# Kernel tuning notes

Measured on AMD Instinct MI355X. Metric: run time of the kernel, lower is better.

## Reference

```python
import jax, jax.numpy as jnp
import numpy as np

N_NODES = 100_000
N_POS = 1_600_000
N_NEG = 1_600_000
HID = 32


def gcn_conv(x, edge_index, W, b, num_nodes):
    """torch_geometric GCNConv: add self-loops, symmetric norm, linear-first, bias after agg."""
    xl = x @ W  # [N, out]
    loops = jnp.arange(num_nodes, dtype=edge_index.dtype)
    src = jnp.concatenate([edge_index[0], loops])
    dst = jnp.concatenate([edge_index[1], loops])
    deg = jax.ops.segment_sum(jnp.ones_like(dst, dtype=xl.dtype), dst, num_segments=num_nodes)
    dinv = jnp.where(deg > 0, jax.lax.rsqrt(deg), 0.0)
    norm = dinv[src] * dinv[dst]  # [E+N]
    out = jax.ops.segment_sum(norm[:, None] * xl[src], dst, num_segments=num_nodes)
    return out + b


def setup_inputs() -> dict:
    key = jax.random.key(0)
    ks = jax.random.split(key, 8)
    x = jax.random.normal(ks[0], (N_NODES, HID), dtype=jnp.float32)
    pos_edge_index = jax.random.randint(ks[1], (2, N_POS), 0, N_NODES, dtype=jnp.int32)
    neg_edge_index = jax.random.randint(ks[2], (2, N_NEG), 0, N_NODES, dtype=jnp.int32)
    s = lambda fan_in: 1.0 / np.sqrt(fan_in)
    W1 = jax.random.normal(ks[3], (HID, 128), dtype=jnp.float32) * s(HID)
    b1 = jnp.zeros((128,), jnp.float32)
    W2 = jax.random.normal(ks[4], (128, HID), dtype=jnp.float32) * s(128)
    b2 = jnp.zeros((HID,), jnp.float32)
    Wm1 = jax.random.normal(ks[5], (2 * HID, HID), dtype=jnp.float32) * s(2 * HID)
    bm1 = jnp.zeros((HID,), jnp.float32)
    Wm2 = jax.random.normal(ks[6], (HID, 2), dtype=jnp.float32) * s(HID)
    bm2 = jnp.zeros((2,), jnp.float32)
    return dict(x=x, pos_edge_index=pos_edge_index, neg_edge_index=neg_edge_index,
                W1=W1, b1=b1, W2=W2, b2=b2, Wm1=Wm1, bm1=bm1, Wm2=Wm2, bm2=bm2)


def reference(x, pos_edge_index, neg_edge_index, W1, b1, W2, b2, Wm1, bm1, Wm2, bm2):
    n = x.shape[0]
    h = jax.nn.relu(gcn_conv(x, pos_edge_index, W1, b1, n))
    h = jax.nn.relu(gcn_conv(h, pos_edge_index, W2, b2, n))  # [N, hid]
    ei = jnp.concatenate([pos_edge_index, neg_edge_index], axis=-1)  # [2, Ep+En]
    feat = jnp.concatenate([h[ei[0]], h[ei[1]]], axis=1)  # [E, 2*hid]
    out = jax.nn.relu(feat @ Wm1 + bm1) @ Wm2 + bm2  # [E, 2]
    return out
```

## Files before the change

kernel.cpp:

```cpp
#include <hip/hip_runtime.h>
#include <hip/hip_fp16.h>


#define HIDN 32
#define SCAN_B 256

struct __align__(8) Half4 { __half2 a, b; };

__global__ void k_deg(const int* __restrict__ dst, int E, int* __restrict__ deg) {
    int e = blockIdx.x * blockDim.x + threadIdx.x;
    if (e < E) atomicAdd(&deg[__builtin_nontemporal_load(dst + e)], 1);
}

__global__ void k_scan1(const int* __restrict__ deg, int N,
                        int* __restrict__ part, int* __restrict__ bsum,
                        float* __restrict__ dinv,
                        const float4* __restrict__ x4, Half4* __restrict__ xs4) {
    __shared__ int sh[SCAN_B];
    __shared__ float dsh[SCAN_B];
    int t = threadIdx.x, i = blockIdx.x * SCAN_B + t;
    int v = (i < N) ? deg[i] : 0;
    float dv = rsqrtf((float)(v + 1));
    if (i < N) dinv[i] = dv;
    dsh[t] = dv;
    sh[t] = v; __syncthreads();
    for (int o = 1; o < SCAN_B; o <<= 1) {
        int a = (t >= o) ? sh[t - o] : 0;
        __syncthreads();
        sh[t] += a;
        __syncthreads();
    }
    if (i < N) part[i] = sh[t] - v;
    if (t == SCAN_B - 1) bsum[blockIdx.x] = sh[t];
#pragma unroll
    for (int it = 0; it < 8; ++it) {
        int q = it * SCAN_B + t;
        int g = blockIdx.x * (SCAN_B * 8) + q;
        if (g < N * 8) {
            float w = dsh[q >> 3];
            float4 a = x4[g];
            Half4 hv;
            hv.a = __floats2half2_rn(a.x * w, a.y * w);
            hv.b = __floats2half2_rn(a.z * w, a.w * w);
            xs4[g] = hv;
        }
    }
}

__global__ void k_scan2(int* __restrict__ bsum, int nb) {
    __shared__ int sh[1024];
    int t = threadIdx.x;
    int v = (t < nb) ? bsum[t] : 0;
    sh[t] = v; __syncthreads();
    for (int o = 1; o < 1024; o <<= 1) {
        int a = (t >= o) ? sh[t - o] : 0;
        __syncthreads();
        sh[t] += a;
        __syncthreads();
    }
    if (t < nb) bsum[t] = sh[t] - v;
}

__global__ void k_scan3(const int* __restrict__ part, const int* __restrict__ bsum,
                        int N, int E, int* __restrict__ rowptr, int* __restrict__ cursor) {
    int i = blockIdx.x * blockDim.x + threadIdx.x;
    if (i < N) {
        int r = part[i] + bsum[i / SCAN_B];
        rowptr[i] = r;
        cursor[i] = r;
    }
    if (i == N) rowptr[N] = E;
}

__global__ void k_fill_sweep(const int* __restrict__ src, const int* __restrict__ dst,
                             int E, int lo, int hi,
                             int* __restrict__ cursor, int* __restrict__ csr) {
    int e = blockIdx.x * blockDim.x + threadIdx.x;
    if (e >= E) return;
    int d = __builtin_nontemporal_load(dst + e);
    if (d >= lo && d < hi) {
        int j = atomicAdd(&cursor[d], 1);
        csr[j] = __builtin_nontemporal_load(src + e);
    }
}

#define ADD8(raw)                                        \
    {                                                    \
        const __half2* _h = (const __half2*)&(raw);      \
        float2 _f;                                       \
        _f = __half22float2(_h[0]); a0 += _f.x; a1 += _f.y; \
        _f = __half22float2(_h[1]); a2 += _f.x; a3 += _f.y; \
        _f = __half22float2(_h[2]); a4 += _f.x; a5 += _f.y; \
        _f = __half22float2(_h[3]); a6 += _f.x; a7 += _f.y; \
    }

__global__ void k_gather_h(const float4* __restrict__ tbl, const float* __restrict__ dinv,
                           const int* __restrict__ rowptr, const int* __restrict__ csr,
                           int N, float4* __restrict__ out) {
    int t = blockIdx.x * blockDim.x + threadIdx.x;
    if (t >= N * 4) return;
    int i = t >> 2, c = t & 3;
    float di = dinv[i];
    float a0 = 0.f, a1 = 0.f, a2 = 0.f, a3 = 0.f;
    float a4 = 0.f, a5 = 0.f, a6 = 0.f, a7 = 0.f;
    {
        float4 raw = tbl[(size_t)i * 4 + c];
        ADD8(raw);
    }
    int p = rowptr[i], end = rowptr[i + 1];
    for (; p + 3 < end; p += 4) {
        int s0 = __builtin_nontemporal_load(csr + p);
        int s1 = __builtin_nontemporal_load(csr + p + 1);
        int s2 = __builtin_nontemporal_load(csr + p + 2);
        int s3 = __builtin_nontemporal_load(csr + p + 3);
        float4 r0 = tbl[(size_t)s0 * 4 + c];
        float4 r1 = tbl[(size_t)s1 * 4 + c];
        float4 r2 = tbl[(size_t)s2 * 4 + c];
        float4 r3 = tbl[(size_t)s3 * 4 + c];
        ADD8(r0); ADD8(r1); ADD8(r2); ADD8(r3);
    }
    for (; p < end; ++p) {
        float4 r = tbl[(size_t)__builtin_nontemporal_load(csr + p) * 4 + c];
        ADD8(r);
    }
    out[(size_t)i * 8 + 2 * c]     = make_float4(a0 * di, a1 * di, a2 * di, a3 * di);
    out[(size_t)i * 8 + 2 * c + 1] = make_float4(a4 * di, a5 * di, a6 * di, a7 * di);
}

__global__ __launch_bounds__(256) void k_mlp1(
        const float4* __restrict__ agg1, const float* __restrict__ dinv,
        const float* __restrict__ W1, const float* __restrict__ b1,
        const float* __restrict__ W2, int N, __half* __restrict__ xl2s) {
    __shared__ float aT[32][65];
    __shared__ __half hT16[64][136];
    int t = threadIdx.x;
    int base = blockIdx.x * 64;
#pragma unroll
    for (int it = 0; it < 2; ++it) {
        int idx = it * 256 + t;
        int n = idx >> 3, q = idx & 7;
        int gi = base + n;
        float4 v = (gi < N) ? agg1[(size_t)gi * 8 + q] : make_float4(0.f, 0.f, 0.f, 0.f);
        aT[q * 4 + 0][n] = v.x; aT[q * 4 + 1][n] = v.y;
        aT[q * 4 + 2][n] = v.z; aT[q * 4 + 3][n] = v.w;
    }
    __syncthreads();
    int j = t & 31, r = t >> 5;
    int n0 = r * 8;
    float acc[8][4];
    {
        float4 bq = *reinterpret_cast<const float4*>(&b1[4 * j]);
#pragma unroll
        for (int n = 0; n < 8; ++n) {
            acc[n][0] = bq.x; acc[n][1] = bq.y; acc[n][2] = bq.z; acc[n][3] = bq.w;
        }
    }
#pragma unroll
    for (int k = 0; k < 32; ++k) {
        float4 w = *reinterpret_cast<const float4*>(&W1[k * 128 + 4 * j]);
#pragma unroll
        for (int n = 0; n < 8; ++n) {
            float a = aT[k][n0 + n];
            acc[n][0] = fmaf(a, w.x, acc[n][0]);
            acc[n][1] = fmaf(a, w.y, acc[n][1]);
            acc[n][2] = fmaf(a, w.z, acc[n][2]);
            acc[n][3] = fmaf(a, w.w, acc[n][3]);
        }
    }
#pragma unroll
    for (int n = 0; n < 8; ++n) {
        Half4 hv;
        hv.a = __floats2half2_rn(fmaxf(acc[n][0], 0.f), fmaxf(acc[n][1], 0.f));
        hv.b = __floats2half2_rn(fmaxf(acc[n][2], 0.f), fmaxf(acc[n][3], 0.f));
        *reinterpret_cast<Half4*>(&hT16[n0 + n][4 * j]) = hv;
    }
    __syncthreads();
    int jo = j & 7, ko = j >> 3;
    float acc2[8][4];
#pragma unroll
    for (int n = 0; n < 8; ++n) { acc2[n][0] = acc2[n][1] = acc2[n][2] = acc2[n][3] = 0.f; }
#pragma unroll
    for (int kk = 0; kk < 8; ++kk) {
        int kbase = ko * 32 + 4 * kk;
        float2 hf[8][2];
#pragma unroll
        for (int n = 0; n < 8; ++n) {
            Half4 hv = *reinterpret_cast<const Half4*>(&hT16[n0 + n][kbase]);
            hf[n][0] = __half22float2(hv.a);
            hf[n][1] = __half22float2(hv.b);
        }
#pragma unroll
        for (int c = 0; c < 4; ++c) {
            float4 w = *reinterpret_cast<const float4*>(&W2[(kbase + c) * 32 + 4 * jo]);
#pragma unroll
            for (int n = 0; n < 8; ++n) {
                float a = (c == 0) ? hf[n][0].x : (c == 1) ? hf[n][0].y
                        : (c == 2) ? hf[n][1].x : hf[n][1].y;
                acc2[n][0] = fmaf(a, w.x, acc2[n][0]);
                acc2[n][1] = fmaf(a, w.y, acc2[n][1]);
                acc2[n][2] = fmaf(a, w.z, acc2[n][2]);
                acc2[n][3] = fmaf(a, w.w, acc2[n][3]);
            }
        }
    }
#pragma unroll
    for (int n = 0; n < 8; ++n)
#pragma unroll
        for (int c = 0; c < 4; ++c) {
            acc2[n][c] += __shfl_xor(acc2[n][c], 8);
            acc2[n][c] += __shfl_xor(acc2[n][c], 16);
        }
    if (ko == 0) {
#pragma unroll
        for (int n = 0; n < 8; ++n) {
            int gi = base + n0 + n;
            if (gi < N) {
                float d = dinv[gi];
                Half4 hv;
                hv.a = __floats2half2_rn(acc2[n][0] * d, acc2[n][1] * d);
                hv.b = __floats2half2_rn(acc2[n][2] * d, acc2[n][3] * d);
                *reinterpret_cast<Half4*>(&xl2s[(size_t)gi * 32 + 4 * jo]) = hv;
            }
        }
    }
}

__global__ __launch_bounds__(256) void k_mlp2(
        const float4* __restrict__ agg2, const float* __restrict__ b2,
        const float* __restrict__ Wm1, int N,
        __half* __restrict__ gt, __half* __restrict__ gb) {
    __shared__ float hT[32][129];
    int t = threadIdx.x;
    int base = blockIdx.x * 128;
    const float4* b2q = reinterpret_cast<const float4*>(b2);
#pragma unroll
    for (int it = 0; it < 4; ++it) {
        int idx = it * 256 + t;
        int n = idx >> 3, q = idx & 7;
        int gi = base + n;
        float4 v = (gi < N) ? agg2[(size_t)gi * 8 + q] : make_float4(0.f, 0.f, 0.f, 0.f);
        float4 bb = b2q[q];
        hT[q * 4 + 0][n] = fmaxf(v.x + bb.x, 0.f);
        hT[q * 4 + 1][n] = fmaxf(v.y + bb.y, 0.f);
        hT[q * 4 + 2][n] = fmaxf(v.z + bb.z, 0.f);
        hT[q * 4 + 3][n] = fmaxf(v.w + bb.w, 0.f);
    }
    __syncthreads();
    int j = t & 15, r = t >> 4;
    int n0 = r * 8;
    int half = j >> 3, jo = j & 7;
    float acc[8][4];
#pragma unroll
    for (int n = 0; n < 8; ++n) { acc[n][0] = acc[n][1] = acc[n][2] = acc[n][3] = 0.f; }
#pragma unroll
    for (int k = 0; k < 32; ++k) {
        float4 w = *reinterpret_cast<const float4*>(&Wm1[(k + half * 32) * 32 + 4 * jo]);
#pragma unroll
        for (int n = 0; n < 8; ++n) {
            float a = hT[k][n0 + n];
            acc[n][0] = fmaf(a, w.x, acc[n][0]);
            acc[n][1] = fmaf(a, w.y, acc[n][1]);
            acc[n][2] = fmaf(a, w.z, acc[n][2]);
            acc[n][3] = fmaf(a, w.w, acc[n][3]);
        }
    }
    __half* dsttab = half ? gb : gt;
#pragma unroll
    for (int n = 0; n < 8; ++n) {
        int gi = base + n0 + n;
        if (gi < N) {
            Half4 hv;
            hv.a = __floats2half2_rn(acc[n][0], acc[n][1]);
            hv.b = __floats2half2_rn(acc[n][2], acc[n][3]);
            *reinterpret_cast<Half4*>(&dsttab[(size_t)gi * 32 + 4 * jo]) = hv;
        }
    }
}

__global__ void k_edge(const int* __restrict__ ps, const int* __restrict__ pd, int Ep,
                       const int* __restrict__ ns, const int* __restrict__ nd, int En,
                       int elo, int ehi,
                       const float4* __restrict__ gt4, const float4* __restrict__ gb4,
                       const float* __restrict__ bm1, const float* __restrict__ Wm2,
                       const float* __restrict__ bm2, float* __restrict__ out) {
    int t = blockIdx.x * blockDim.x + threadIdx.x;
    int p = t >> 2, q = t & 3;
    int cnt = ehi - elo;
    int Pc = (cnt + 1) >> 1;
    if (p >= Pc) return;
    int e0 = elo + p, e1 = elo + p + Pc;
    int u0, v0;
    if (e0 < Ep) { u0 = __builtin_nontemporal_load(ps + e0); v0 = __builtin_nontemporal_load(pd + e0); }
    else         { u0 = __builtin_nontemporal_load(ns + (e0 - Ep)); v0 = __builtin_nontemporal_load(nd + (e0 - Ep)); }
    bool has1 = (e1 < ehi);
    int u1 = u0, v1 = v0;
    if (has1) {
        if (e1 < Ep) { u1 = __builtin_nontemporal_load(ps + e1); v1 = __builtin_nontemporal_load(pd + e1); }
        else         { u1 = __builtin_nontemporal_load(ns + (e1 - Ep)); v1 = __builtin_nontemporal_load(nd + (e1 - Ep)); }
    }
    float4 a0raw = gt4[(size_t)u0 * 4 + q];
    float4 b0raw = gb4[(size_t)v0 * 4 + q];
    float4 a1raw = gt4[(size_t)u1 * 4 + q];
    float4 b1raw = gb4[(size_t)v1 * 4 + q];
    const __half* a0h = (const __half*)&a0raw;
    const __half* b0h = (const __half*)&b0raw;
    const __half* a1h = (const __half*)&a1raw;
    const __half* b1h = (const __half*)&b1raw;
    int k0 = q * 8;
    float o00 = 0.f, o01 = 0.f, o10 = 0.f, o11 = 0.f;
#pragma unroll
    for (int r = 0; r < 8; ++r) {
        float bm = bm1[k0 + r];
        float w0 = Wm2[(k0 + r) * 2 + 0];
        float w1 = Wm2[(k0 + r) * 2 + 1];
        float h0 = fmaxf(__half2float(a0h[r]) + __half2float(b0h[r]) + bm, 0.f);
        o00 = fmaf(h0, w0, o00); o01 = fmaf(h0, w1, o01);
        float h1 = fmaxf(__half2float(a1h[r]) + __half2float(b1h[r]) + bm, 0.f);
        o10 = fmaf(h1, w0, o10); o11 = fmaf(h1, w1, o11);
    }
    o00 += __shfl_down(o00, 2, 4); o01 += __shfl_down(o01, 2, 4);
    o00 += __shfl_down(o00, 1, 4); o01 += __shfl_down(o01, 1, 4);
    o10 += __shfl_down(o10, 2, 4); o11 += __shfl_down(o11, 2, 4);
    o10 += __shfl_down(o10, 1, 4); o11 += __shfl_down(o11, 1, 4);
    if (q == 0) {
        float c0 = bm2[0], c1 = bm2[1];
        __builtin_nontemporal_store(o00 + c0, out + (size_t)e0 * 2 + 0);
        __builtin_nontemporal_store(o01 + c1, out + (size_t)e0 * 2 + 1);
        if (has1) {
            __builtin_nontemporal_store(o10 + c0, out + (size_t)e1 * 2 + 0);
            __builtin_nontemporal_store(o11 + c1, out + (size_t)e1 * 2 + 1);
        }
    }
}

extern "C" void kernel_launch(void* const* d_in, const int* in_sizes, int n_in,
                              void* d_out, int out_size, void* d_ws, size_t ws_size,
                              hipStream_t stream) {
    const float* x   = (const float*)d_in[0];
    const int*   pei = (const int*)d_in[1];
    const int*   nei = (const int*)d_in[2];
    const float* W1  = (const float*)d_in[3];
    const float* b1  = (const float*)d_in[4];
    const float* W2  = (const float*)d_in[5];
    const float* b2  = (const float*)d_in[6];
    const float* Wm1 = (const float*)d_in[7];
    const float* bm1 = (const float*)d_in[8];
    const float* Wm2 = (const float*)d_in[9];
    const float* bm2 = (const float*)d_in[10];

    const int N  = in_sizes[0] / HIDN;
    const int Ep = in_sizes[1] / 2;
    const int En = in_sizes[2] / 2;
    const int* ps = pei;
    const int* pd = pei + Ep;
    const int* ns = nei;
    const int* nd = nei + En;
    const int nb = (N + SCAN_B - 1) / SCAN_B;

    char* ws = (char*)d_ws;
    size_t off = 0;
    auto alloc = [&](size_t bytes) { size_t o = off; off += (bytes + 255) & ~(size_t)255; return o; };
    int*    deg    = (int*)(ws + alloc((size_t)N * 4));
    float*  dinv   = (float*)(ws + alloc((size_t)N * 4));
    int*    part   = (int*)(ws + alloc((size_t)N * 4));
    int*    bsum   = (int*)(ws + alloc((size_t)1024 * 4));
    int*    rowptr = (int*)(ws + alloc((size_t)(N + 1) * 4));
    int*    cursor = (int*)(ws + alloc((size_t)N * 4));
    int*    csr    = (int*)(ws + alloc((size_t)Ep * 4));
    __half* xs     = (__half*)(ws + alloc((size_t)N * HIDN * 2));
    float*  agg1   = (float*)(ws + alloc((size_t)N * HIDN * 4));
    __half* xl2s   = (__half*)(ws + alloc((size_t)N * HIDN * 2));
    float*  agg2   = (float*)(ws + alloc((size_t)N * HIDN * 4));
    __half* gt     = (__half*)(ws + alloc((size_t)N * HIDN * 2));
    __half* gb     = (__half*)(ws + alloc((size_t)N * HIDN * 2));

    hipMemsetAsync(deg, 0, (size_t)N * 4, stream);
    k_deg<<<(Ep + 255) / 256, 256, 0, stream>>>(pd, Ep, deg);
    k_scan1<<<nb, SCAN_B, 0, stream>>>(deg, N, part, bsum, dinv,
                                       (const float4*)x, (Half4*)xs);
    k_scan2<<<1, 1024, 0, stream>>>(bsum, nb);
    k_scan3<<<(N + 256) / 256, 256, 0, stream>>>(part, bsum, N, Ep, rowptr, cursor);
    {
        int grid = (Ep + 255) / 256;
        for (int s = 0; s < 4; ++s) {
            int lo = (int)((size_t)N * s / 4);
            int hi = (int)((size_t)N * (s + 1) / 4);
            k_fill_sweep<<<grid, 256, 0, stream>>>(ps, pd, Ep, lo, hi, cursor, csr);
        }
    }

    k_gather_h<<<(N * 4 + 255) / 256, 256, 0, stream>>>(
        (const float4*)xs, dinv, rowptr, csr, N, (float4*)agg1);
    k_mlp1<<<(N + 63) / 64, 256, 0, stream>>>(
        (const float4*)agg1, dinv, W1, b1, W2, N, xl2s);

    k_gather_h<<<(N * 4 + 255) / 256, 256, 0, stream>>>(
        (const float4*)xl2s, dinv, rowptr, csr, N, (float4*)agg2);
    k_mlp2<<<(N + 127) / 128, 256, 0, stream>>>(
        (const float4*)agg2, b2, Wm1, N, gt, gb);

    {
        int E = Ep + En;
        for (int c = 0; c < 3; ++c) {
            int elo = (int)((size_t)E * c / 3);
            int ehi = (int)((size_t)E * (c + 1) / 3);
            int cnt = ehi - elo;
            int Pc = (cnt + 1) / 2;
            size_t threads = (size_t)Pc * 4;
            k_edge<<<(int)((threads + 255) / 256), 256, 0, stream>>>(
                ps, pd, Ep, ns, nd, En, elo, ehi,
                (const float4*)gt, (const float4*)gb,
                bm1, Wm2, bm2, (float*)d_out);
        }
    }
}
```

Baseline: 380.8 us.

## Shard degree and cursor atomics eight ways and merge edge MLP launches

```diff
diff --git a/kernel.cpp b/kernel.cpp
--- a/kernel.cpp
+++ b/kernel.cpp
@@ -7,19 +7,24 @@
 
 struct __align__(8) Half4 { __half2 a, b; };
 
-__global__ void k_deg(const int* __restrict__ dst, int E, int* __restrict__ deg) {
+__global__ void k_deg(const int* __restrict__ dst, int E, int N, int* __restrict__ deg8) {
     int e = blockIdx.x * blockDim.x + threadIdx.x;
-    if (e < E) atomicAdd(&deg[__builtin_nontemporal_load(dst + e)], 1);
-}
-
-__global__ void k_scan1(const int* __restrict__ deg, int N,
+    if (e < E)
+        atomicAdd(&deg8[(size_t)(e & 7) * N + __builtin_nontemporal_load(dst + e)], 1);
+}
+
+__global__ void k_scan1(const int* __restrict__ deg8, int N,
                         int* __restrict__ part, int* __restrict__ bsum,
                         float* __restrict__ dinv,
                         const float4* __restrict__ x4, Half4* __restrict__ xs4) {
     __shared__ int sh[SCAN_B];
     __shared__ float dsh[SCAN_B];
     int t = threadIdx.x, i = blockIdx.x * SCAN_B + t;
-    int v = (i < N) ? deg[i] : 0;
+    int v = 0;
+    if (i < N) {
+#pragma unroll
+        for (int c = 0; c < 8; ++c) v += deg8[(size_t)c * N + i];
+    }
     float dv = rsqrtf((float)(v + 1));
     if (i < N) dinv[i] = dv;
     dsh[t] = dv;
@@ -62,24 +67,30 @@
 }
 
 __global__ void k_scan3(const int* __restrict__ part, const int* __restrict__ bsum,
-                        int N, int E, int* __restrict__ rowptr, int* __restrict__ cursor) {
+                        const int* __restrict__ deg8,
+                        int N, int E, int* __restrict__ rowptr, int* __restrict__ cursor8) {
     int i = blockIdx.x * blockDim.x + threadIdx.x;
     if (i < N) {
         int r = part[i] + bsum[i / SCAN_B];
         rowptr[i] = r;
-        cursor[i] = r;
+        int base = r;
+#pragma unroll
+        for (int c = 0; c < 8; ++c) {
+            cursor8[(size_t)c * N + i] = base;
+            base += deg8[(size_t)c * N + i];
+        }
     }
     if (i == N) rowptr[N] = E;
 }
 
 __global__ void k_fill_sweep(const int* __restrict__ src, const int* __restrict__ dst,
-                             int E, int lo, int hi,
-                             int* __restrict__ cursor, int* __restrict__ csr) {
+                             int E, int N, int lo, int hi,
+                             int* __restrict__ cursor8, int* __restrict__ csr) {
     int e = blockIdx.x * blockDim.x + threadIdx.x;
     if (e >= E) return;
     int d = __builtin_nontemporal_load(dst + e);
     if (d >= lo && d < hi) {
-        int j = atomicAdd(&cursor[d], 1);
+        int j = atomicAdd(&cursor8[(size_t)(e & 7) * N + d], 1);
         csr[j] = __builtin_nontemporal_load(src + e);
     }
 }
@@ -279,20 +290,19 @@
 
 __global__ void k_edge(const int* __restrict__ ps, const int* __restrict__ pd, int Ep,
                        const int* __restrict__ ns, const int* __restrict__ nd, int En,
-                       int elo, int ehi,
+                       int P,
                        const float4* __restrict__ gt4, const float4* __restrict__ gb4,
                        const float* __restrict__ bm1, const float* __restrict__ Wm2,
                        const float* __restrict__ bm2, float* __restrict__ out) {
     int t = blockIdx.x * blockDim.x + threadIdx.x;
     int p = t >> 2, q = t & 3;
-    int cnt = ehi - elo;
-    int Pc = (cnt + 1) >> 1;
-    if (p >= Pc) return;
-    int e0 = elo + p, e1 = elo + p + Pc;
+    if (p >= P) return;
+    int E = Ep + En;
+    int e0 = p, e1 = p + P;
     int u0, v0;
     if (e0 < Ep) { u0 = __builtin_nontemporal_load(ps + e0); v0 = __builtin_nontemporal_load(pd + e0); }
     else         { u0 = __builtin_nontemporal_load(ns + (e0 - Ep)); v0 = __builtin_nontemporal_load(nd + (e0 - Ep)); }
-    bool has1 = (e1 < ehi);
+    bool has1 = (e1 < E);
     int u1 = u0, v1 = v0;
     if (has1) {
         if (e1 < Ep) { u1 = __builtin_nontemporal_load(ps + e1); v1 = __builtin_nontemporal_load(pd + e1); }
@@ -360,32 +370,32 @@
     char* ws = (char*)d_ws;
     size_t off = 0;
     auto alloc = [&](size_t bytes) { size_t o = off; off += (bytes + 255) & ~(size_t)255; return o; };
-    int*    deg    = (int*)(ws + alloc((size_t)N * 4));
-    float*  dinv   = (float*)(ws + alloc((size_t)N * 4));
-    int*    part   = (int*)(ws + alloc((size_t)N * 4));
-    int*    bsum   = (int*)(ws + alloc((size_t)1024 * 4));
-    int*    rowptr = (int*)(ws + alloc((size_t)(N + 1) * 4));
-    int*    cursor = (int*)(ws + alloc((size_t)N * 4));
-    int*    csr    = (int*)(ws + alloc((size_t)Ep * 4));
-    __half* xs     = (__half*)(ws + alloc((size_t)N * HIDN * 2));
-    float*  agg1   = (float*)(ws + alloc((size_t)N * HIDN * 4));
-    __half* xl2s   = (__half*)(ws + alloc((size_t)N * HIDN * 2));
-    float*  agg2   = (float*)(ws + alloc((size_t)N * HIDN * 4));
-    __half* gt     = (__half*)(ws + alloc((size_t)N * HIDN * 2));
-    __half* gb     = (__half*)(ws + alloc((size_t)N * HIDN * 2));
-
-    hipMemsetAsync(deg, 0, (size_t)N * 4, stream);
-    k_deg<<<(Ep + 255) / 256, 256, 0, stream>>>(pd, Ep, deg);
-    k_scan1<<<nb, SCAN_B, 0, stream>>>(deg, N, part, bsum, dinv,
+    int*    deg8    = (int*)(ws + alloc((size_t)N * 8 * 4));
+    int*    cursor8 = (int*)(ws + alloc((size_t)N * 8 * 4));
+    float*  dinv    = (float*)(ws + alloc((size_t)N * 4));
+    int*    part    = (int*)(ws + alloc((size_t)N * 4));
+    int*    bsum    = (int*)(ws + alloc((size_t)1024 * 4));
+    int*    rowptr  = (int*)(ws + alloc((size_t)(N + 1) * 4));
+    int*    csr     = (int*)(ws + alloc((size_t)Ep * 4));
+    __half* xs      = (__half*)(ws + alloc((size_t)N * HIDN * 2));
+    float*  agg1    = (float*)(ws + alloc((size_t)N * HIDN * 4));
+    __half* xl2s    = (__half*)(ws + alloc((size_t)N * HIDN * 2));
+    float*  agg2    = (float*)(ws + alloc((size_t)N * HIDN * 4));
+    __half* gt      = (__half*)(ws + alloc((size_t)N * HIDN * 2));
+    __half* gb      = (__half*)(ws + alloc((size_t)N * HIDN * 2));
+
+    hipMemsetAsync(deg8, 0, (size_t)N * 8 * 4, stream);
+    k_deg<<<(Ep + 255) / 256, 256, 0, stream>>>(pd, Ep, N, deg8);
+    k_scan1<<<nb, SCAN_B, 0, stream>>>(deg8, N, part, bsum, dinv,
                                        (const float4*)x, (Half4*)xs);
     k_scan2<<<1, 1024, 0, stream>>>(bsum, nb);
-    k_scan3<<<(N + 256) / 256, 256, 0, stream>>>(part, bsum, N, Ep, rowptr, cursor);
+    k_scan3<<<(N + 256) / 256, 256, 0, stream>>>(part, bsum, deg8, N, Ep, rowptr, cursor8);
     {
         int grid = (Ep + 255) / 256;
         for (int s = 0; s < 4; ++s) {
             int lo = (int)((size_t)N * s / 4);
             int hi = (int)((size_t)N * (s + 1) / 4);
-            k_fill_sweep<<<grid, 256, 0, stream>>>(ps, pd, Ep, lo, hi, cursor, csr);
+            k_fill_sweep<<<grid, 256, 0, stream>>>(ps, pd, Ep, N, lo, hi, cursor8, csr);
         }
     }
 
@@ -401,16 +411,11 @@
 
     {
         int E = Ep + En;
-        for (int c = 0; c < 3; ++c) {
-            int elo = (int)((size_t)E * c / 3);
-            int ehi = (int)((size_t)E * (c + 1) / 3);
-            int cnt = ehi - elo;
-            int Pc = (cnt + 1) / 2;
-            size_t threads = (size_t)Pc * 4;
-            k_edge<<<(int)((threads + 255) / 256), 256, 0, stream>>>(
-                ps, pd, Ep, ns, nd, En, elo, ehi,
-                (const float4*)gt, (const float4*)gb,
-                bm1, Wm2, bm2, (float*)d_out);
-        }
-    }
-}
+        int P = (E + 1) / 2;
+        size_t threads = (size_t)P * 4;
+        k_edge<<<(int)((threads + 255) / 256), 256, 0, stream>>>(
+            ps, pd, Ep, ns, nd, En, P,
+            (const float4*)gt, (const float4*)gb,
+            bm1, Wm2, bm2, (float*)d_out);
+    }
+}
```

New measurement: 362.5 us. 1.05x faster.
